# Kernel tuning notes

Hardware: AMD Instinct MI355X
Metric: run time of the kernel (lower is better)

Reference implementation:

```python
import jax, jax.numpy as jnp
import numpy as np

N_HEADS = 16
HIDDEN = 1024
HEAD = HIDDEN // N_HEADS


def setup_inputs() -> dict:
    key = jax.random.key(0)
    ks = jax.random.split(key, 11)
    B, S, H = 2, 2048, HIDDEN
    s = 1.0 / np.sqrt(H)
    return {
        "query": jax.random.normal(ks[0], (B, S, H), jnp.float32),
        "key": jax.random.normal(ks[1], (B, S, H), jnp.float32),
        "value": jax.random.normal(ks[2], (B, S, H), jnp.float32),
        "Wq": jax.random.normal(ks[3], (H, H), jnp.float32) * s,
        "bq": jnp.zeros((H,), jnp.float32),
        "Wk": jax.random.normal(ks[4], (H, H), jnp.float32) * s,
        "bk": jnp.zeros((H,), jnp.float32),
        "Wv": jax.random.normal(ks[5], (H, H), jnp.float32) * s,
        "bv": jnp.zeros((H,), jnp.float32),
        "Wo": jax.random.normal(ks[6], (H, H), jnp.float32) * s,
        "bo": jnp.zeros((H,), jnp.float32),
    }


def reference(query, key, value, Wq, bq, Wk, bk, Wv, bv, Wo, bo):
    B, Sq, H = query.shape
    Sk = key.shape[1]
    # QKV projections, split heads: [B, n_heads, S, head]
    q = (query @ Wq + bq).reshape(B, Sq, N_HEADS, HEAD).transpose(0, 2, 1, 3)
    k = (key @ Wk + bk).reshape(B, Sk, N_HEADS, HEAD).transpose(0, 2, 1, 3)
    v = (value @ Wv + bv).reshape(B, Sk, N_HEADS, HEAD).transpose(0, 2, 1, 3)
    # scaled dot-product attention (no mask, dropout p=0)
    scores = jnp.einsum("bhqd,bhkd->bhqk", q, k) / np.sqrt(HEAD).astype(np.float32)
    attn = jax.nn.softmax(scores, axis=-1)
    out = jnp.einsum("bhqk,bhkd->bhqd", attn, v)
    out = out.transpose(0, 2, 1, 3).reshape(B, Sq, H)
    return out @ Wo + bo
```

## Files before the change

### kernel.cpp

```cpp
#include <hip/hip_runtime.h>
#include <hip/hip_bf16.h>
#include <stdint.h>

typedef unsigned short u16;
typedef short bf16x8 __attribute__((ext_vector_type(8)));
typedef float f32x4 __attribute__((ext_vector_type(4)));

#define DEVI static __device__ __forceinline__

#if __has_builtin(__builtin_amdgcn_exp2f)
#define EXP2F(x) __builtin_amdgcn_exp2f(x)
#else
#define EXP2F(x) exp2f(x)
#endif

DEVI u16 f2bf(float f) {
  union { float f; uint32_t u; } v; v.f = f;
  uint32_t u = v.u;
  u += 0x7fffu + ((u >> 16) & 1u);
  return (u16)(u >> 16);
}
DEVI uint32_t pk2bf(float lo, float hi) {
  __hip_bfloat162 h = __float22bfloat162_rn(float2{lo, hi});
  union { __hip_bfloat162 h; uint32_t u; } v; v.h = h; return v.u;
}

DEVI void async16(const void* g, const void* l) {
  __builtin_amdgcn_global_load_lds(
      (const __attribute__((address_space(1))) void*)g,
      (__attribute__((address_space(3))) void*)l, 16, 0, 0);
}

DEVI f32x4 mfma16(bf16x8 a, bf16x8 b, f32x4 c) {
  return __builtin_amdgcn_mfma_f32_16x16x32_bf16(a, b, c, 0, 0, 0);
}

#define CSC 0.18033688011112042f

__global__ void convx(const float* __restrict__ q, const float* __restrict__ k,
                      const float* __restrict__ v, u16* __restrict__ out) {
  const int z = blockIdx.y;
  const float* src = (z == 0) ? q : (z == 1) ? k : v;
  const int i = (blockIdx.x * 256 + threadIdx.x) * 4;
  float4 f = *(const float4*)(src + i);
  ushort4 o;
  o.x = f2bf(f.x); o.y = f2bf(f.y); o.z = f2bf(f.z); o.w = f2bf(f.w);
  *(ushort4*)(out + (size_t)z * 4194304 + i) = o;
}

__global__ void transw(const float* __restrict__ Wq, const float* __restrict__ Wk,
                       const float* __restrict__ Wv, const float* __restrict__ Wo,
                       u16* __restrict__ WT) {
  __shared__ u16 tile[64 * 68];
  const int z = blockIdx.z;
  const float* W = (z == 0) ? Wq : (z == 1) ? Wk : (z == 2) ? Wv : Wo;
  u16* out = WT + (size_t)z * 1048576;
  const int R0 = blockIdx.y * 64, C0 = blockIdx.x * 64;
  const int t = threadIdx.x;
#pragma unroll
  for (int it = 0; it < 16; ++it) {
    int j = it * 256 + t;
    int r = j >> 6, c = j & 63;
    tile[r * 68 + c] = f2bf(W[(size_t)(R0 + r) * 1024 + C0 + c]);
  }
  __syncthreads();
#pragma unroll
  for (int it = 0; it < 16; ++it) {
    int j = it * 256 + t;
    int c = j >> 6, r = j & 63;
    out[(size_t)(C0 + c) * 1024 + R0 + r] = tile[r * 68 + c];
  }
}

__global__ __launch_bounds__(256, 3)
void qkv_gemm(const u16* __restrict__ XB, const u16* __restrict__ WT,
              const float* __restrict__ bq, const float* __restrict__ bk,
              const float* __restrict__ bv,
              u16* __restrict__ QH, u16* __restrict__ KH, u16* __restrict__ VT) {
  __shared__ u16 lA[128 * 64];
  __shared__ u16 lB[128 * 64];
  const int z = blockIdx.z;
  const u16* A  = XB + (size_t)z * 4194304;
  const u16* Bt = WT + (size_t)z * 1048576;
  const float* bias = (z == 0) ? bq : (z == 1) ? bk : bv;
  const int t = threadIdx.x, lane = t & 63, w = t >> 6;
  const int quad = lane >> 4, l16 = lane & 15;
  const int wm = (w & 1) * 64, wn = (w >> 1) * 64;
  const int n0 = blockIdx.x * 128, m0 = blockIdx.y * 128;

  f32x4 acc[4][4] = {};
  for (int kt = 0; kt < 16; ++kt) {
    const int k0 = kt * 64;
#pragma unroll
    for (int it = 0; it < 4; ++it) {
      int i = it * 256 + t;
      int r = i >> 3, cc = i & 7, c = cc ^ (r & 7);
      async16(A + (size_t)(m0 + r) * 1024 + k0 + c * 8, &lA[i * 8]);
      async16(Bt + (size_t)(n0 + r) * 1024 + k0 + c * 8, &lB[i * 8]);
    }
    __syncthreads();
#pragma unroll
    for (int ks = 0; ks < 2; ++ks) {
      bf16x8 af[4], bfr[4];
#pragma unroll
      for (int rt = 0; rt < 4; ++rt) {
        int row = wm + rt * 16 + l16;
        af[rt] = *(const bf16x8*)&lA[row * 64 + ((ks * 4 + quad) ^ (row & 7)) * 8];
      }
#pragma unroll
      for (int ct = 0; ct < 4; ++ct) {
        int row = wn + ct * 16 + l16;
        bfr[ct] = *(const bf16x8*)&lB[row * 64 + ((ks * 4 + quad) ^ (row & 7)) * 8];
      }
#pragma unroll
      for (int rt = 0; rt < 4; ++rt)
#pragma unroll
        for (int ct = 0; ct < 4; ++ct)
          acc[rt][ct] = mfma16(af[rt], bfr[ct], acc[rt][ct]);
    }
    __syncthreads();
  }

  float bvv[4];
  int ncol[4];
#pragma unroll
  for (int ct = 0; ct < 4; ++ct) {
    ncol[ct] = n0 + wn + ct * 16 + l16;
    bvv[ct] = bias[ncol[ct]];
  }
  if (z < 2) {
    u16* out = (z == 0) ? QH : KH;
    const float scl = (z == 0) ? CSC : 1.0f;
#pragma unroll
    for (int rt = 0; rt < 4; ++rt)
#pragma unroll
      for (int r = 0; r < 4; ++r) {
        int m = m0 + wm + rt * 16 + quad * 4 + r;
        int bb = m >> 11, s = m & 2047;
#pragma unroll
        for (int ct = 0; ct < 4; ++ct) {
          int hh = ncol[ct] >> 6, d = ncol[ct] & 63;
          out[((size_t)((bb * 16 + hh) * 2048 + s)) * 64 + d] =
              f2bf((acc[rt][ct][r] + bvv[ct]) * scl);
        }
      }
  } else {
#pragma unroll
    for (int rt = 0; rt < 4; ++rt) {
      int mb = m0 + wm + rt * 16 + quad * 4;
      int bb = mb >> 11, sb = mb & 2047;
#pragma unroll
      for (int ct = 0; ct < 4; ++ct) {
        int hh = ncol[ct] >> 6, d = ncol[ct] & 63;
        ushort4 pk;
        pk.x = f2bf(acc[rt][ct][0] + bvv[ct]);
        pk.y = f2bf(acc[rt][ct][1] + bvv[ct]);
        pk.z = f2bf(acc[rt][ct][2] + bvv[ct]);
        pk.w = f2bf(acc[rt][ct][3] + bvv[ct]);
        *(ushort4*)&VT[((size_t)((bb * 16 + hh) * 64 + d)) * 2048 + sb] = pk;
      }
    }
  }
}

__global__ __launch_bounds__(512, 4)
void attn3(const u16* __restrict__ QH, const u16* __restrict__ KH,
           const u16* __restrict__ VT, u16* __restrict__ AO) {
  __shared__ u16 lK[2][64 * 64];
  __shared__ u16 lV[2][64 * 64];
  __shared__ u16 lPT[8][16 * 72];
  const int qt0 = blockIdx.x, h = blockIdx.y, b = blockIdx.z;
  const int t = threadIdx.x, lane = t & 63, w = t >> 6;
  const int quad = lane >> 4, l16 = lane & 15;
  const u16* Qg = QH + ((size_t)((b * 16 + h) * 2048 + qt0 * 128)) * 64;
  const u16* Kg = KH + ((size_t)((b * 16 + h) * 2048)) * 64;
  const u16* Vg = VT + ((size_t)((b * 16 + h) * 64)) * 2048;

  bf16x8 qf[2];
#pragma unroll
  for (int ks = 0; ks < 2; ++ks)
    qf[ks] = *(const bf16x8*)(Qg + (size_t)(w * 16 + l16) * 64 + ks * 32 + quad * 8);

  {
    int r = t >> 3, cc = t & 7, c = cc ^ (r & 7);
    async16(Kg + (size_t)r * 64 + c * 8, &lK[0][t * 8]);
    async16(Vg + (size_t)r * 2048 + c * 8, &lV[0][t * 8]);
  }
  __syncthreads();

  f32x4 o[4] = {};
  float lsum = 0.f;
  u16* myP = &lPT[w][0];

  for (int kt = 0; kt < 32; ++kt) {
    const int cur = kt & 1, nxt = cur ^ 1;
    if (kt + 1 < 32) {
      const int kb = (kt + 1) * 64;
      int r = t >> 3, cc = t & 7, c = cc ^ (r & 7);
      async16(Kg + (size_t)(kb + r) * 64 + c * 8, &lK[nxt][t * 8]);
      async16(Vg + (size_t)r * 2048 + kb + c * 8, &lV[nxt][t * 8]);
    }

    f32x4 sc[4];
#pragma unroll
    for (int st = 0; st < 4; ++st) {
      int row = st * 16 + l16;
      bf16x8 kf0 = *(const bf16x8*)&lK[cur][row * 64 + ((quad) ^ (row & 7)) * 8];
      bf16x8 kf1 = *(const bf16x8*)&lK[cur][row * 64 + ((4 + quad) ^ (row & 7)) * 8];
      f32x4 z = {};
      sc[st] = mfma16(kf0, qf[0], z);
      sc[st] = mfma16(kf1, qf[1], sc[st]);
    }

#pragma unroll
    for (int st = 0; st < 4; ++st) {
      float p0 = EXP2F(sc[st][0]);
      float p1 = EXP2F(sc[st][1]);
      float p2 = EXP2F(sc[st][2]);
      float p3 = EXP2F(sc[st][3]);
      lsum += (p0 + p1) + (p2 + p3);
      uint2 pk;
      pk.x = pk2bf(p0, p1);
      pk.y = pk2bf(p2, p3);
      *(uint2*)&myP[l16 * 72 + st * 16 + quad * 4] = pk;
    }

#pragma unroll
    for (int ks2 = 0; ks2 < 2; ++ks2) {
      bf16x8 pf = *(const bf16x8*)&myP[l16 * 72 + ks2 * 32 + quad * 8];
#pragma unroll
      for (int dt = 0; dt < 4; ++dt) {
        int row = dt * 16 + l16;
        bf16x8 vf = *(const bf16x8*)&lV[cur][row * 64 + ((ks2 * 4 + quad) ^ (row & 7)) * 8];
        o[dt] = mfma16(vf, pf, o[dt]);
      }
    }
    __syncthreads();
  }

  float l = lsum;
  l += __shfl_xor(l, 16, 64);
  l += __shfl_xor(l, 32, 64);
  float inv = 1.0f / l;
  int qglob = qt0 * 128 + w * 16 + l16;
  size_t base = ((size_t)(b * 2048 + qglob)) * 1024 + h * 64;
#pragma unroll
  for (int dt = 0; dt < 4; ++dt) {
    ushort4 pk;
    pk.x = f2bf(o[dt][0] * inv);
    pk.y = f2bf(o[dt][1] * inv);
    pk.z = f2bf(o[dt][2] * inv);
    pk.w = f2bf(o[dt][3] * inv);
    *(ushort4*)&AO[base + dt * 16 + quad * 4] = pk;
  }
}

__global__ __launch_bounds__(256, 2)
void oproj_gemm(const u16* __restrict__ AO, const u16* __restrict__ Bt,
                const float* __restrict__ bias, float* __restrict__ out) {
  __shared__ u16 lA[128 * 64];
  __shared__ u16 lB[64 * 64];
  const int t = threadIdx.x, lane = t & 63, w = t >> 6;
  const int quad = lane >> 4, l16 = lane & 15;
  const int wm = (w & 1) * 64, wn = (w >> 1) * 32;
  const int n0 = blockIdx.x * 64, m0 = blockIdx.y * 128;

  f32x4 acc[4][2] = {};
  for (int kt = 0; kt < 16; ++kt) {
    const int k0 = kt * 64;
#pragma unroll
    for (int it = 0; it < 4; ++it) {
      int i = it * 256 + t;
      int r = i >> 3, cc = i & 7, c = cc ^ (r & 7);
      async16(AO + (size_t)(m0 + r) * 1024 + k0 + c * 8, &lA[i * 8]);
    }
#pragma unroll
    for (int it = 0; it < 2; ++it) {
      int i = it * 256 + t;
      int r = i >> 3, cc = i & 7, c = cc ^ (r & 7);
      async16(Bt + (size_t)(n0 + r) * 1024 + k0 + c * 8, &lB[i * 8]);
    }
    __syncthreads();
#pragma unroll
    for (int ks = 0; ks < 2; ++ks) {
      bf16x8 af[4], bfr[2];
#pragma unroll
      for (int rt = 0; rt < 4; ++rt) {
        int row = wm + rt * 16 + l16;
        af[rt] = *(const bf16x8*)&lA[row * 64 + ((ks * 4 + quad) ^ (row & 7)) * 8];
      }
#pragma unroll
      for (int ct = 0; ct < 2; ++ct) {
        int row = wn + ct * 16 + l16;
        bfr[ct] = *(const bf16x8*)&lB[row * 64 + ((ks * 4 + quad) ^ (row & 7)) * 8];
      }
#pragma unroll
      for (int rt = 0; rt < 4; ++rt)
#pragma unroll
        for (int ct = 0; ct < 2; ++ct)
          acc[rt][ct] = mfma16(af[rt], bfr[ct], acc[rt][ct]);
    }
    __syncthreads();
  }

#pragma unroll
  for (int ct = 0; ct < 2; ++ct) {
    int ncol = n0 + wn + ct * 16 + l16;
    float bvv = bias[ncol];
#pragma unroll
    for (int rt = 0; rt < 4; ++rt)
#pragma unroll
      for (int r = 0; r < 4; ++r) {
        int m = m0 + wm + rt * 16 + quad * 4 + r;
        out[(size_t)m * 1024 + ncol] = acc[rt][ct][r] + bvv;
      }
  }
}

extern "C" void kernel_launch(void* const* d_in, const int* in_sizes, int n_in,
                              void* d_out, int out_size, void* d_ws, size_t ws_size,
                              hipStream_t stream) {
  const float* query = (const float*)d_in[0];
  const float* key   = (const float*)d_in[1];
  const float* value = (const float*)d_in[2];
  const float* Wq = (const float*)d_in[3];
  const float* bq = (const float*)d_in[4];
  const float* Wk = (const float*)d_in[5];
  const float* bk = (const float*)d_in[6];
  const float* Wv = (const float*)d_in[7];
  const float* bv = (const float*)d_in[8];
  const float* Wo = (const float*)d_in[9];
  const float* bo = (const float*)d_in[10];
  float* out = (float*)d_out;

  u16* WT = (u16*)d_ws;
  u16* QH = WT + 4 * 1048576;
  u16* KH = QH + 4194304;
  u16* VT = KH + 4194304;
  u16* XB = VT + 4194304;
  u16* AO = XB;

  convx<<<dim3(4096, 3), 256, 0, stream>>>(query, key, value, XB);
  transw<<<dim3(16, 16, 4), 256, 0, stream>>>(Wq, Wk, Wv, Wo, WT);
  qkv_gemm<<<dim3(8, 32, 3), 256, 0, stream>>>(XB, WT, bq, bk, bv, QH, KH, VT);
  attn3<<<dim3(16, 16, 2), 512, 0, stream>>>(QH, KH, VT, AO);
  oproj_gemm<<<dim3(16, 32), 256, 0, stream>>>(AO, WT + 3 * 1048576, bo, out);
}
```

Before: 222.7 us.

## Give each attention warp two query tiles and vectorize GEMM epilogue stores

The attention kernel now runs with 256 threads and each warp handles two 16-row query tiles. Each K/V fragment read from LDS is reused for twice as many MFMAs, which lowers LDS traffic per unit of work at the cost of more registers per thread. In the Q/K projection and output-projection GEMMs, the MFMA operands are swapped so each lane holds four consecutive columns. This lets the epilogues do vectorized bias loads and packed ushort4/float4 stores instead of scalar scattered writes.

```diff
diff --git a/kernel.cpp b/kernel.cpp
--- a/kernel.cpp
+++ b/kernel.cpp
@@ -112,38 +112,43 @@
         int row = wn + ct * 16 + l16;
         bfr[ct] = *(const bf16x8*)&lB[row * 64 + ((ks * 4 + quad) ^ (row & 7)) * 8];
       }
-#pragma unroll
-      for (int rt = 0; rt < 4; ++rt)
-#pragma unroll
-        for (int ct = 0; ct < 4; ++ct)
-          acc[rt][ct] = mfma16(af[rt], bfr[ct], acc[rt][ct]);
-    }
-    __syncthreads();
-  }
-
-  float bvv[4];
-  int ncol[4];
-#pragma unroll
-  for (int ct = 0; ct < 4; ++ct) {
-    ncol[ct] = n0 + wn + ct * 16 + l16;
-    bvv[ct] = bias[ncol[ct]];
-  }
+      if (z < 2) {
+#pragma unroll
+        for (int rt = 0; rt < 4; ++rt)
+#pragma unroll
+          for (int ct = 0; ct < 4; ++ct)
+            acc[rt][ct] = mfma16(bfr[ct], af[rt], acc[rt][ct]);
+      } else {
+#pragma unroll
+        for (int rt = 0; rt < 4; ++rt)
+#pragma unroll
+          for (int ct = 0; ct < 4; ++ct)
+            acc[rt][ct] = mfma16(af[rt], bfr[ct], acc[rt][ct]);
+      }
+    }
+    __syncthreads();
+  }
+
   if (z < 2) {
     u16* out = (z == 0) ? QH : KH;
     const float scl = (z == 0) ? CSC : 1.0f;
 #pragma unroll
-    for (int rt = 0; rt < 4; ++rt)
-#pragma unroll
-      for (int r = 0; r < 4; ++r) {
-        int m = m0 + wm + rt * 16 + quad * 4 + r;
-        int bb = m >> 11, s = m & 2047;
-#pragma unroll
-        for (int ct = 0; ct < 4; ++ct) {
-          int hh = ncol[ct] >> 6, d = ncol[ct] & 63;
-          out[((size_t)((bb * 16 + hh) * 2048 + s)) * 64 + d] =
-              f2bf((acc[rt][ct][r] + bvv[ct]) * scl);
-        }
-      }
+    for (int rt = 0; rt < 4; ++rt) {
+      int mm = m0 + wm + rt * 16 + l16;
+      int bb = mm >> 11, s = mm & 2047;
+#pragma unroll
+      for (int ct = 0; ct < 4; ++ct) {
+        int nb = n0 + wn + ct * 16 + quad * 4;
+        int hh = nb >> 6, d = nb & 63;
+        float4 b4 = *(const float4*)&bias[nb];
+        ushort4 pk;
+        pk.x = f2bf((acc[rt][ct][0] + b4.x) * scl);
+        pk.y = f2bf((acc[rt][ct][1] + b4.y) * scl);
+        pk.z = f2bf((acc[rt][ct][2] + b4.z) * scl);
+        pk.w = f2bf((acc[rt][ct][3] + b4.w) * scl);
+        *(ushort4*)&out[((size_t)((bb * 16 + hh) * 2048 + s)) * 64 + d] = pk;
+      }
+    }
   } else {
 #pragma unroll
     for (int rt = 0; rt < 4; ++rt) {
@@ -151,24 +156,26 @@
       int bb = mb >> 11, sb = mb & 2047;
 #pragma unroll
       for (int ct = 0; ct < 4; ++ct) {
-        int hh = ncol[ct] >> 6, d = ncol[ct] & 63;
+        int ncol = n0 + wn + ct * 16 + l16;
+        int hh = ncol >> 6, d = ncol & 63;
+        float bvv = bias[ncol];
         ushort4 pk;
-        pk.x = f2bf(acc[rt][ct][0] + bvv[ct]);
-        pk.y = f2bf(acc[rt][ct][1] + bvv[ct]);
-        pk.z = f2bf(acc[rt][ct][2] + bvv[ct]);
-        pk.w = f2bf(acc[rt][ct][3] + bvv[ct]);
+        pk.x = f2bf(acc[rt][ct][0] + bvv);
+        pk.y = f2bf(acc[rt][ct][1] + bvv);
+        pk.z = f2bf(acc[rt][ct][2] + bvv);
+        pk.w = f2bf(acc[rt][ct][3] + bvv);
         *(ushort4*)&VT[((size_t)((bb * 16 + hh) * 64 + d)) * 2048 + sb] = pk;
       }
     }
   }
 }
 
-__global__ __launch_bounds__(512, 4)
-void attn3(const u16* __restrict__ QH, const u16* __restrict__ KH,
+__global__ __launch_bounds__(256, 2)
+void attn4(const u16* __restrict__ QH, const u16* __restrict__ KH,
            const u16* __restrict__ VT, u16* __restrict__ AO) {
   __shared__ u16 lK[2][64 * 64];
   __shared__ u16 lV[2][64 * 64];
-  __shared__ u16 lPT[8][16 * 72];
+  __shared__ u16 lPT[4][32 * 72];
   const int qt0 = blockIdx.x, h = blockIdx.y, b = blockIdx.z;
   const int t = threadIdx.x, lane = t & 63, w = t >> 6;
   const int quad = lane >> 4, l16 = lane & 15;
@@ -176,82 +183,102 @@
   const u16* Kg = KH + ((size_t)((b * 16 + h) * 2048)) * 64;
   const u16* Vg = VT + ((size_t)((b * 16 + h) * 64)) * 2048;
 
-  bf16x8 qf[2];
-#pragma unroll
-  for (int ks = 0; ks < 2; ++ks)
-    qf[ks] = *(const bf16x8*)(Qg + (size_t)(w * 16 + l16) * 64 + ks * 32 + quad * 8);
-
-  {
-    int r = t >> 3, cc = t & 7, c = cc ^ (r & 7);
-    async16(Kg + (size_t)r * 64 + c * 8, &lK[0][t * 8]);
-    async16(Vg + (size_t)r * 2048 + c * 8, &lV[0][t * 8]);
+  bf16x8 qf[2][2];
+#pragma unroll
+  for (int qt = 0; qt < 2; ++qt)
+#pragma unroll
+    for (int ks = 0; ks < 2; ++ks)
+      qf[qt][ks] = *(const bf16x8*)(Qg + (size_t)(w * 32 + qt * 16 + l16) * 64 +
+                                    ks * 32 + quad * 8);
+
+#pragma unroll
+  for (int it = 0; it < 2; ++it) {
+    int s = it * 256 + t;
+    int r = s >> 3, cc = s & 7, c = cc ^ (r & 7);
+    async16(Kg + (size_t)r * 64 + c * 8, &lK[0][s * 8]);
+    async16(Vg + (size_t)r * 2048 + c * 8, &lV[0][s * 8]);
   }
   __syncthreads();
 
-  f32x4 o[4] = {};
-  float lsum = 0.f;
+  f32x4 o[2][4] = {};
+  float lsum[2] = {0.f, 0.f};
   u16* myP = &lPT[w][0];
 
   for (int kt = 0; kt < 32; ++kt) {
     const int cur = kt & 1, nxt = cur ^ 1;
     if (kt + 1 < 32) {
       const int kb = (kt + 1) * 64;
-      int r = t >> 3, cc = t & 7, c = cc ^ (r & 7);
-      async16(Kg + (size_t)(kb + r) * 64 + c * 8, &lK[nxt][t * 8]);
-      async16(Vg + (size_t)r * 2048 + kb + c * 8, &lV[nxt][t * 8]);
-    }
-
-    f32x4 sc[4];
+#pragma unroll
+      for (int it = 0; it < 2; ++it) {
+        int s = it * 256 + t;
+        int r = s >> 3, cc = s & 7, c = cc ^ (r & 7);
+        async16(Kg + (size_t)(kb + r) * 64 + c * 8, &lK[nxt][s * 8]);
+        async16(Vg + (size_t)r * 2048 + kb + c * 8, &lV[nxt][s * 8]);
+      }
+    }
+
+    f32x4 sc[2][4];
 #pragma unroll
     for (int st = 0; st < 4; ++st) {
       int row = st * 16 + l16;
       bf16x8 kf0 = *(const bf16x8*)&lK[cur][row * 64 + ((quad) ^ (row & 7)) * 8];
       bf16x8 kf1 = *(const bf16x8*)&lK[cur][row * 64 + ((4 + quad) ^ (row & 7)) * 8];
       f32x4 z = {};
-      sc[st] = mfma16(kf0, qf[0], z);
-      sc[st] = mfma16(kf1, qf[1], sc[st]);
-    }
-
-#pragma unroll
-    for (int st = 0; st < 4; ++st) {
-      float p0 = EXP2F(sc[st][0]);
-      float p1 = EXP2F(sc[st][1]);
-      float p2 = EXP2F(sc[st][2]);
-      float p3 = EXP2F(sc[st][3]);
-      lsum += (p0 + p1) + (p2 + p3);
-      uint2 pk;
-      pk.x = pk2bf(p0, p1);
-      pk.y = pk2bf(p2, p3);
-      *(uint2*)&myP[l16 * 72 + st * 16 + quad * 4] = pk;
+      sc[0][st] = mfma16(kf0, qf[0][0], z);
+      sc[0][st] = mfma16(kf1, qf[0][1], sc[0][st]);
+      sc[1][st] = mfma16(kf0, qf[1][0], z);
+      sc[1][st] = mfma16(kf1, qf[1][1], sc[1][st]);
+    }
+
+#pragma unroll
+    for (int qt = 0; qt < 2; ++qt) {
+      int prow = qt * 16 + l16;
+#pragma unroll
+      for (int st = 0; st < 4; ++st) {
+        float p0 = EXP2F(sc[qt][st][0]);
+        float p1 = EXP2F(sc[qt][st][1]);
+        float p2 = EXP2F(sc[qt][st][2]);
+        float p3 = EXP2F(sc[qt][st][3]);
+        lsum[qt] += (p0 + p1) + (p2 + p3);
+        uint2 pk;
+        pk.x = pk2bf(p0, p1);
+        pk.y = pk2bf(p2, p3);
+        *(uint2*)&myP[prow * 72 + st * 16 + quad * 4] = pk;
+      }
     }
 
 #pragma unroll
     for (int ks2 = 0; ks2 < 2; ++ks2) {
-      bf16x8 pf = *(const bf16x8*)&myP[l16 * 72 + ks2 * 32 + quad * 8];
+      bf16x8 pf0 = *(const bf16x8*)&myP[(l16) * 72 + ks2 * 32 + quad * 8];
+      bf16x8 pf1 = *(const bf16x8*)&myP[(16 + l16) * 72 + ks2 * 32 + quad * 8];
 #pragma unroll
       for (int dt = 0; dt < 4; ++dt) {
         int row = dt * 16 + l16;
         bf16x8 vf = *(const bf16x8*)&lV[cur][row * 64 + ((ks2 * 4 + quad) ^ (row & 7)) * 8];
-        o[dt] = mfma16(vf, pf, o[dt]);
-      }
-    }
-    __syncthreads();
-  }
-
-  float l = lsum;
-  l += __shfl_xor(l, 16, 64);
-  l += __shfl_xor(l, 32, 64);
-  float inv = 1.0f / l;
-  int qglob = qt0 * 128 + w * 16 + l16;
-  size_t base = ((size_t)(b * 2048 + qglob)) * 1024 + h * 64;
-#pragma unroll
-  for (int dt = 0; dt < 4; ++dt) {
-    ushort4 pk;
-    pk.x = f2bf(o[dt][0] * inv);
-    pk.y = f2bf(o[dt][1] * inv);
-    pk.z = f2bf(o[dt][2] * inv);
-    pk.w = f2bf(o[dt][3] * inv);
-    *(ushort4*)&AO[base + dt * 16 + quad * 4] = pk;
+        o[0][dt] = mfma16(vf, pf0, o[0][dt]);
+        o[1][dt] = mfma16(vf, pf1, o[1][dt]);
+      }
+    }
+    __syncthreads();
+  }
+
+#pragma unroll
+  for (int qt = 0; qt < 2; ++qt) {
+    float l = lsum[qt];
+    l += __shfl_xor(l, 16, 64);
+    l += __shfl_xor(l, 32, 64);
+    float inv = 1.0f / l;
+    int qglob = qt0 * 128 + w * 32 + qt * 16 + l16;
+    size_t base = ((size_t)(b * 2048 + qglob)) * 1024 + h * 64;
+#pragma unroll
+    for (int dt = 0; dt < 4; ++dt) {
+      ushort4 pk;
+      pk.x = f2bf(o[qt][dt][0] * inv);
+      pk.y = f2bf(o[qt][dt][1] * inv);
+      pk.z = f2bf(o[qt][dt][2] * inv);
+      pk.w = f2bf(o[qt][dt][3] * inv);
+      *(ushort4*)&AO[base + dt * 16 + quad * 4] = pk;
+    }
   }
 }
 
@@ -298,22 +325,25 @@
       for (int rt = 0; rt < 4; ++rt)
 #pragma unroll
         for (int ct = 0; ct < 2; ++ct)
-          acc[rt][ct] = mfma16(af[rt], bfr[ct], acc[rt][ct]);
-    }
-    __syncthreads();
-  }
-
-#pragma unroll
-  for (int ct = 0; ct < 2; ++ct) {
-    int ncol = n0 + wn + ct * 16 + l16;
-    float bvv = bias[ncol];
-#pragma unroll
-    for (int rt = 0; rt < 4; ++rt)
-#pragma unroll
-      for (int r = 0; r < 4; ++r) {
-        int m = m0 + wm + rt * 16 + quad * 4 + r;
-        out[(size_t)m * 1024 + ncol] = acc[rt][ct][r] + bvv;
-      }
+          acc[rt][ct] = mfma16(bfr[ct], af[rt], acc[rt][ct]);
+    }
+    __syncthreads();
+  }
+
+#pragma unroll
+  for (int rt = 0; rt < 4; ++rt) {
+    int m = m0 + wm + rt * 16 + l16;
+#pragma unroll
+    for (int ct = 0; ct < 2; ++ct) {
+      int nb = n0 + wn + ct * 16 + quad * 4;
+      float4 b4 = *(const float4*)&bias[nb];
+      float4 st;
+      st.x = acc[rt][ct][0] + b4.x;
+      st.y = acc[rt][ct][1] + b4.y;
+      st.z = acc[rt][ct][2] + b4.z;
+      st.w = acc[rt][ct][3] + b4.w;
+      *(float4*)&out[(size_t)m * 1024 + nb] = st;
+    }
   }
 }
 
@@ -343,6 +373,6 @@
   convx<<<dim3(4096, 3), 256, 0, stream>>>(query, key, value, XB);
   transw<<<dim3(16, 16, 4), 256, 0, stream>>>(Wq, Wk, Wv, Wo, WT);
   qkv_gemm<<<dim3(8, 32, 3), 256, 0, stream>>>(XB, WT, bq, bk, bv, QH, KH, VT);
-  attn3<<<dim3(16, 16, 2), 512, 0, stream>>>(QH, KH, VT, AO);
+  attn4<<<dim3(16, 16, 2), 256, 0, stream>>>(QH, KH, VT, AO);
   oproj_gemm<<<dim3(16, 32), 256, 0, stream>>>(AO, WT + 3 * 1048576, bo, out);
 }
```

After: 285.3 us. 28.1% more time.

## Stage QKV epilogue through LDS for coalesced stores and use row-major Q/K

Applied to the files above, without the earlier changes.

The QKV GEMM epilogue now writes bias-added bf16 results into shared memory first (transposed for V), then issues 16-byte coalesced global stores instead of scattered 2-byte or 8-byte writes. Q and K are kept in plain [B*S, 1024] row-major layout, and the attention kernel reads them with a 1024 stride rather than a head-major layout. Both GEMM grids are flattened so that consecutive blocks share the same weight column tile, which should improve L2 reuse. The price is an extra LDS round trip and barrier in the epilogue, plus strided per-head Q/K loads in attention.

```diff
diff --git a/kernel.cpp b/kernel.cpp
--- a/kernel.cpp
+++ b/kernel.cpp
@@ -76,17 +76,19 @@
 void qkv_gemm(const u16* __restrict__ XB, const u16* __restrict__ WT,
               const float* __restrict__ bq, const float* __restrict__ bk,
               const float* __restrict__ bv,
-              u16* __restrict__ QH, u16* __restrict__ KH, u16* __restrict__ VT) {
-  __shared__ u16 lA[128 * 64];
-  __shared__ u16 lB[128 * 64];
-  const int z = blockIdx.z;
+              u16* __restrict__ QN, u16* __restrict__ KN, u16* __restrict__ VT) {
+  __shared__ u16 smem[16896];
+  u16* lA = smem;
+  u16* lB = smem + 8192;
+  const int z = blockIdx.y;
   const u16* A  = XB + (size_t)z * 4194304;
   const u16* Bt = WT + (size_t)z * 1048576;
   const float* bias = (z == 0) ? bq : (z == 1) ? bk : bv;
+  const int T = blockIdx.x;
+  const int m0 = (T & 31) * 128, n0 = (T >> 5) * 128;
   const int t = threadIdx.x, lane = t & 63, w = t >> 6;
   const int quad = lane >> 4, l16 = lane & 15;
   const int wm = (w & 1) * 64, wn = (w >> 1) * 64;
-  const int n0 = blockIdx.x * 128, m0 = blockIdx.y * 128;
 
   f32x4 acc[4][4] = {};
   for (int kt = 0; kt < 16; ++kt) {
@@ -116,55 +118,66 @@
       for (int rt = 0; rt < 4; ++rt)
 #pragma unroll
         for (int ct = 0; ct < 4; ++ct)
-          acc[rt][ct] = mfma16(af[rt], bfr[ct], acc[rt][ct]);
-    }
-    __syncthreads();
-  }
-
-  float bvv[4];
-  int ncol[4];
-#pragma unroll
-  for (int ct = 0; ct < 4; ++ct) {
-    ncol[ct] = n0 + wn + ct * 16 + l16;
-    bvv[ct] = bias[ncol[ct]];
-  }
+          acc[rt][ct] = mfma16(bfr[ct], af[rt], acc[rt][ct]);
+    }
+    __syncthreads();
+  }
+
   if (z < 2) {
-    u16* out = (z == 0) ? QH : KH;
     const float scl = (z == 0) ? CSC : 1.0f;
 #pragma unroll
-    for (int rt = 0; rt < 4; ++rt)
-#pragma unroll
-      for (int r = 0; r < 4; ++r) {
-        int m = m0 + wm + rt * 16 + quad * 4 + r;
-        int bb = m >> 11, s = m & 2047;
-#pragma unroll
-        for (int ct = 0; ct < 4; ++ct) {
-          int hh = ncol[ct] >> 6, d = ncol[ct] & 63;
-          out[((size_t)((bb * 16 + hh) * 2048 + s)) * 64 + d] =
-              f2bf((acc[rt][ct][r] + bvv[ct]) * scl);
-        }
-      }
+    for (int rt = 0; rt < 4; ++rt) {
+      int sl = wm + rt * 16 + l16;
+#pragma unroll
+      for (int ct = 0; ct < 4; ++ct) {
+        int nb = wn + ct * 16 + quad * 4;
+        float4 b4 = *(const float4*)&bias[n0 + nb];
+        ushort4 pk;
+        pk.x = f2bf((acc[rt][ct][0] + b4.x) * scl);
+        pk.y = f2bf((acc[rt][ct][1] + b4.y) * scl);
+        pk.z = f2bf((acc[rt][ct][2] + b4.z) * scl);
+        pk.w = f2bf((acc[rt][ct][3] + b4.w) * scl);
+        *(ushort4*)&smem[sl * 132 + nb] = pk;
+      }
+    }
+    __syncthreads();
+    u16* out = (z == 0) ? QN : KN;
+#pragma unroll
+    for (int p = 0; p < 8; ++p) {
+      int idx = p * 256 + t;
+      int row = idx >> 4, chunk = idx & 15;
+      *(bf16x8*)&out[(size_t)(m0 + row) * 1024 + n0 + chunk * 8] =
+          *(const bf16x8*)&smem[row * 132 + chunk * 8];
+    }
   } else {
 #pragma unroll
     for (int rt = 0; rt < 4; ++rt) {
-      int mb = m0 + wm + rt * 16 + quad * 4;
-      int bb = mb >> 11, sb = mb & 2047;
+      int sl = wm + rt * 16 + l16;
 #pragma unroll
       for (int ct = 0; ct < 4; ++ct) {
-        int hh = ncol[ct] >> 6, d = ncol[ct] & 63;
-        ushort4 pk;
-        pk.x = f2bf(acc[rt][ct][0] + bvv[ct]);
-        pk.y = f2bf(acc[rt][ct][1] + bvv[ct]);
-        pk.z = f2bf(acc[rt][ct][2] + bvv[ct]);
-        pk.w = f2bf(acc[rt][ct][3] + bvv[ct]);
-        *(ushort4*)&VT[((size_t)((bb * 16 + hh) * 64 + d)) * 2048 + sb] = pk;
-      }
+        int nb = wn + ct * 16 + quad * 4;
+        float4 b4 = *(const float4*)&bias[n0 + nb];
+        smem[(nb + 0) * 132 + sl] = f2bf(acc[rt][ct][0] + b4.x);
+        smem[(nb + 1) * 132 + sl] = f2bf(acc[rt][ct][1] + b4.y);
+        smem[(nb + 2) * 132 + sl] = f2bf(acc[rt][ct][2] + b4.z);
+        smem[(nb + 3) * 132 + sl] = f2bf(acc[rt][ct][3] + b4.w);
+      }
+    }
+    __syncthreads();
+    const int bb = m0 >> 11, sb = m0 & 2047;
+#pragma unroll
+    for (int p = 0; p < 8; ++p) {
+      int idx = p * 256 + t;
+      int dl = idx >> 4, chunk = idx & 15;
+      int ncol = n0 + dl, hh = ncol >> 6, dd = ncol & 63;
+      *(bf16x8*)&VT[((size_t)((bb * 16 + hh) * 64 + dd)) * 2048 + sb + chunk * 8] =
+          *(const bf16x8*)&smem[dl * 132 + chunk * 8];
     }
   }
 }
 
 __global__ __launch_bounds__(512, 4)
-void attn3(const u16* __restrict__ QH, const u16* __restrict__ KH,
+void attn5(const u16* __restrict__ QN, const u16* __restrict__ KN,
            const u16* __restrict__ VT, u16* __restrict__ AO) {
   __shared__ u16 lK[2][64 * 64];
   __shared__ u16 lV[2][64 * 64];
@@ -172,18 +185,18 @@
   const int qt0 = blockIdx.x, h = blockIdx.y, b = blockIdx.z;
   const int t = threadIdx.x, lane = t & 63, w = t >> 6;
   const int quad = lane >> 4, l16 = lane & 15;
-  const u16* Qg = QH + ((size_t)((b * 16 + h) * 2048 + qt0 * 128)) * 64;
-  const u16* Kg = KH + ((size_t)((b * 16 + h) * 2048)) * 64;
+  const u16* Qg = QN + ((size_t)(b * 2048 + qt0 * 128)) * 1024 + h * 64;
+  const u16* Kg = KN + ((size_t)b * 2048) * 1024 + h * 64;
   const u16* Vg = VT + ((size_t)((b * 16 + h) * 64)) * 2048;
 
   bf16x8 qf[2];
 #pragma unroll
   for (int ks = 0; ks < 2; ++ks)
-    qf[ks] = *(const bf16x8*)(Qg + (size_t)(w * 16 + l16) * 64 + ks * 32 + quad * 8);
+    qf[ks] = *(const bf16x8*)(Qg + (size_t)(w * 16 + l16) * 1024 + ks * 32 + quad * 8);
 
   {
     int r = t >> 3, cc = t & 7, c = cc ^ (r & 7);
-    async16(Kg + (size_t)r * 64 + c * 8, &lK[0][t * 8]);
+    async16(Kg + (size_t)r * 1024 + c * 8, &lK[0][t * 8]);
     async16(Vg + (size_t)r * 2048 + c * 8, &lV[0][t * 8]);
   }
   __syncthreads();
@@ -197,7 +210,7 @@
     if (kt + 1 < 32) {
       const int kb = (kt + 1) * 64;
       int r = t >> 3, cc = t & 7, c = cc ^ (r & 7);
-      async16(Kg + (size_t)(kb + r) * 64 + c * 8, &lK[nxt][t * 8]);
+      async16(Kg + (size_t)(kb + r) * 1024 + c * 8, &lK[nxt][t * 8]);
       async16(Vg + (size_t)r * 2048 + kb + c * 8, &lV[nxt][t * 8]);
     }
 
@@ -260,10 +273,11 @@
                 const float* __restrict__ bias, float* __restrict__ out) {
   __shared__ u16 lA[128 * 64];
   __shared__ u16 lB[64 * 64];
+  const int T = blockIdx.x;
+  const int m0 = (T & 31) * 128, n0 = (T >> 5) * 64;
   const int t = threadIdx.x, lane = t & 63, w = t >> 6;
   const int quad = lane >> 4, l16 = lane & 15;
   const int wm = (w & 1) * 64, wn = (w >> 1) * 32;
-  const int n0 = blockIdx.x * 64, m0 = blockIdx.y * 128;
 
   f32x4 acc[4][2] = {};
   for (int kt = 0; kt < 16; ++kt) {
@@ -334,15 +348,15 @@
   float* out = (float*)d_out;
 
   u16* WT = (u16*)d_ws;
-  u16* QH = WT + 4 * 1048576;
-  u16* KH = QH + 4194304;
-  u16* VT = KH + 4194304;
+  u16* QN = WT + 4 * 1048576;
+  u16* KN = QN + 4194304;
+  u16* VT = KN + 4194304;
   u16* XB = VT + 4194304;
   u16* AO = XB;
 
   convx<<<dim3(4096, 3), 256, 0, stream>>>(query, key, value, XB);
   transw<<<dim3(16, 16, 4), 256, 0, stream>>>(Wq, Wk, Wv, Wo, WT);
-  qkv_gemm<<<dim3(8, 32, 3), 256, 0, stream>>>(XB, WT, bq, bk, bv, QH, KH, VT);
-  attn3<<<dim3(16, 16, 2), 512, 0, stream>>>(QH, KH, VT, AO);
-  oproj_gemm<<<dim3(16, 32), 256, 0, stream>>>(AO, WT + 3 * 1048576, bo, out);
-}
+  qkv_gemm<<<dim3(256, 3), 256, 0, stream>>>(XB, WT, bq, bk, bv, QN, KN, VT);
+  attn5<<<dim3(16, 16, 2), 512, 0, stream>>>(QN, KN, VT, AO);
+  oproj_gemm<<<dim3(512), 256, 0, stream>>>(AO, WT + 3 * 1048576, bo, out);
+}
```

Measured after the change: 218.7 us. No clear change (-1.8%).
